# Kernel tuning notes

Hardware: AMD Instinct MI355X
Metric: run time of the kernel (lower is better)

## Reference

```python
import jax, jax.numpy as jnp
import numpy as np

IN_FEATURES = 512
OUT_FEATURES = 512
GRID_MIN = -2.0
GRID_MAX = 2.0
NUM_GRIDS = 8
SPLINE_SCALE = 0.1
BATCH = 16384


def setup_inputs() -> dict:
    key = jax.random.key(0)
    kx, kw = jax.random.split(key)
    x = jax.random.normal(kx, (BATCH, IN_FEATURES), dtype=jnp.float32)
    grid = jnp.linspace(GRID_MIN, GRID_MAX, NUM_GRIDS, dtype=jnp.float32)
    spline_weight = (
        jax.random.normal(kw, (IN_FEATURES * NUM_GRIDS, OUT_FEATURES), dtype=jnp.float32)
        * SPLINE_SCALE
    )
    return {"x": x, "grid": grid, "spline_weight": spline_weight}


def reference(x, grid, spline_weight):
    # denominator h = (grid_max - grid_min) / (num_grids - 1)
    h = (GRID_MAX - GRID_MIN) / (NUM_GRIDS - 1)
    # basis: [B, in_features, num_grids]
    basis = jnp.exp(-jnp.square((x[..., None] - grid) / h))
    # flatten to [B, in_features * num_grids] and GEMM
    return basis.reshape(basis.shape[0], -1) @ spline_weight
```

## Files before the change

### kernel.cpp

```cpp
#include <hip/hip_runtime.h>
#include <hip/hip_bf16.h>

#define BATCH 16384
#define IN_F 512
#define OUT_F 512
#define NG 8
#define KTOT (IN_F * NG)

#define SH    2.1019642153762872f
#define SSTEP 1.2011224087864498f
#define BC0N  4.2039284307525745f
#define RC1   2.4022448175728996f

typedef __attribute__((ext_vector_type(8))) short short8;
typedef __attribute__((ext_vector_type(16))) float f32x16;
typedef __attribute__((ext_vector_type(4))) float f32x4;
typedef __attribute__((ext_vector_type(2))) float f32x2;
typedef __attribute__((ext_vector_type(4))) unsigned int u32x4;
typedef __attribute__((ext_vector_type(2))) unsigned int u32x2;

__device__ __forceinline__ unsigned fbits(float f) {
    union { float f; unsigned u; } v; v.f = f; return v.u;
}
__device__ __forceinline__ unsigned pack2bf(float lo, float hi) {
    return __builtin_amdgcn_perm(fbits(hi) + 0x8000u, fbits(lo) + 0x8000u,
                                 0x07060302u);
}
__device__ __forceinline__ unsigned cvtpk(float lo, float hi) {
    unsigned r;
    asm("v_cvt_pk_bf16_f32 %0, %1, %2" : "=v"(r) : "v"(lo), "v"(hi));
    return r;
}

__device__ __forceinline__ short8 basis_frag(float x) {
    const float t0  = fmaf(x, SH, BC0N);
    const float rho = __builtin_amdgcn_exp2f(t0 * RC1);
    const float v0  = __builtin_amdgcn_exp2f(-t0 * t0);
    const float v1 = v0 * rho;
    const float v2 = v1 * rho;
    const float v3 = v2 * rho;
    const float v4 = v3 * rho;
    const float v5 = v4 * rho;
    const float v6 = v5 * rho;
    const float v7 = v6 * rho;
    u32x4 pk;
    pk[0] = cvtpk(v0, v1);
    pk[1] = cvtpk(v2, v3);
    pk[2] = cvtpk(v4, v5);
    pk[3] = cvtpk(v6, v7);
    union { u32x4 u; short8 s; } cv; cv.u = pk;
    return cv.s;
}

__global__ void prep14(const float* __restrict__ W, const float* __restrict__ X,
                       unsigned short* __restrict__ Wt32, float* __restrict__ XtF32) {
    const int tid = threadIdx.x;
    if (blockIdx.x < 1024) {
        const int gid  = blockIdx.x * 256 + tid;
        const int lane = gid & 63;
        const int t    = (gid >> 6) & 255;
        const int s32  = gid >> 14;
        const int n    = s32 * 32 + (lane & 31);
        const int k0   = t * 16 + (lane >> 5) * 8;
        constexpr float QS[8] = {1.0f,
                                 3.6787944117144233e-1f,
                                 1.8315638888734179e-2f,
                                 1.2340980408667956e-4f,
                                 1.1253517471925912e-7f,
                                 1.3887943864964021e-11f,
                                 2.3195228302435693e-16f,
                                 5.2428856633634640e-22f};
        u32x4 pk;
#pragma unroll
        for (int e = 0; e < 4; ++e)
            pk[e] = pack2bf(W[(size_t)(k0 + 2 * e) * OUT_F + n] * QS[2 * e],
                            W[(size_t)(k0 + 2 * e + 1) * OUT_F + n] * QS[2 * e + 1]);
        *(u32x4*)(Wt32 + (size_t)gid * 8) = pk;
    } else {
        __shared__ float ls[64][36];
        const int bid2 = blockIdx.x - 1024;
        const int rb   = bid2 >> 4;
        const int g    = bid2 & 15;
        const int m0   = rb * 64;
        const int c0   = g * 32;
#pragma unroll
        for (int p = 0; p < 2; ++p) {
            const int idx  = p * 1024 + tid * 4;
            const int row  = idx >> 5;
            const int col4 = idx & 31;
            f32x4 v = *(const f32x4*)(X + (size_t)(m0 + row) * IN_F + c0 + col4);
            *(f32x4*)(&ls[row][col4]) = v;
        }
        __syncthreads();
#pragma unroll
        for (int q = 0; q < 4; ++q) {
            const int p    = q * 256 + tid;
            const int th   = p >> 6;
            const int lane = p & 63;
            const int col  = th * 2 + (lane >> 5);
            f32x2 v;
            v.x = ls[lane & 31][col];
            v.y = ls[(lane & 31) + 32][col];
            *(f32x2*)(XtF32 + ((size_t)(rb * 256 + g * 16 + th) * 64 + lane) * 2) = v;
        }
    }
}

__global__ __launch_bounds__(256, 2) void gauss_gemm14(
        const float* __restrict__ XtF32, const unsigned short* __restrict__ Wt32,
        float* __restrict__ Out) {
    const int tid  = threadIdx.x;
    const int lane = tid & 63;
    const int wave = tid >> 6;
    const int nb = (blockIdx.x & 7) * 64 + (blockIdx.x >> 3);
    const int cb = nb >> 8;
    const int rb = nb & 255;
    const int m0 = rb * 64;
    const int n0 = cb * 256;
    const int s64 = cb * 4 + wave;
    const int s32a = s64 * 2, s32b = s64 * 2 + 1;

    const unsigned short* bp0 = Wt32 + (size_t)s32a * 131072 + lane * 8;
    const unsigned short* bp1 = Wt32 + (size_t)s32b * 131072 + lane * 8;
    const float* ap = XtF32 + (size_t)rb * 32768 + lane * 2;

    f32x16 c00 = {0.f}, c01 = {0.f}, c10 = {0.f}, c11 = {0.f};
#pragma unroll
    for (int e = 0; e < 16; ++e) { c00[e] = 0.f; c01[e] = 0.f; c10[e] = 0.f; c11[e] = 0.f; }

    short8 b0C, b1C, b0N, b1N;
    f32x2 xC, xN;

    xC  = *(const f32x2*)(ap);
    b0C = *(const short8*)(bp0);
    b1C = *(const short8*)(bp1);

#define GG14(XU, B0U, B1U, XF, B0F, B1F, DOFF)                                 \
    {                                                                          \
        XF  = *(const f32x2*)(ap + (DOFF) * 128);                              \
        B0F = *(const short8*)(bp0 + (DOFF) * 512);                            \
        B1F = *(const short8*)(bp1 + (DOFF) * 512);                            \
        const short8 a0 = basis_frag(XU.x);                                    \
        const short8 a1 = basis_frag(XU.y);                                    \
        __builtin_amdgcn_s_setprio(1);                                         \
        c00 = __builtin_amdgcn_mfma_f32_32x32x16_bf16(a0, B0U, c00, 0, 0, 0);  \
        c01 = __builtin_amdgcn_mfma_f32_32x32x16_bf16(a0, B1U, c01, 0, 0, 0);  \
        c10 = __builtin_amdgcn_mfma_f32_32x32x16_bf16(a1, B0U, c10, 0, 0, 0);  \
        c11 = __builtin_amdgcn_mfma_f32_32x32x16_bf16(a1, B1U, c11, 0, 0, 0);  \
        __builtin_amdgcn_s_setprio(0);                                         \
    }

    for (int m = 0; m < 127; ++m) {
        GG14(xC, b0C, b1C, xN, b0N, b1N, 1)
        GG14(xN, b0N, b1N, xC, b0C, b1C, 2)
        ap  += 256;
        bp0 += 1024;
        bp1 += 1024;
    }
    GG14(xC, b0C, b1C, xN, b0N, b1N, 1)
    {
        const short8 a0 = basis_frag(xN.x);
        const short8 a1 = basis_frag(xN.y);
        __builtin_amdgcn_s_setprio(1);
        c00 = __builtin_amdgcn_mfma_f32_32x32x16_bf16(a0, b0N, c00, 0, 0, 0);
        c01 = __builtin_amdgcn_mfma_f32_32x32x16_bf16(a0, b1N, c01, 0, 0, 0);
        c10 = __builtin_amdgcn_mfma_f32_32x32x16_bf16(a1, b0N, c10, 0, 0, 0);
        c11 = __builtin_amdgcn_mfma_f32_32x32x16_bf16(a1, b1N, c11, 0, 0, 0);
        __builtin_amdgcn_s_setprio(0);
    }
#undef GG14

    const int ccol = lane & 31;
    const int rof  = 4 * (lane >> 5);
#pragma unroll
    for (int e = 0; e < 16; ++e) {
        const int row = (e & 3) + 8 * (e >> 2) + rof;
        const int c0c = n0 + wave * 64 + ccol;
        Out[(size_t)(m0 + row) * OUT_F + c0c]            = c00[e];
        Out[(size_t)(m0 + row) * OUT_F + c0c + 32]       = c01[e];
        Out[(size_t)(m0 + 32 + row) * OUT_F + c0c]       = c10[e];
        Out[(size_t)(m0 + 32 + row) * OUT_F + c0c + 32]  = c11[e];
    }
}

#define BM 128
#define BN 128
#define BK 64
#define LDA 72
#define LDB 72

__global__ __launch_bounds__(256, 2) void gauss_gemm_fb(
        const float* __restrict__ X, const float* __restrict__ W,
        float* __restrict__ Out) {
    __shared__ __align__(16) unsigned short sA[BM * LDA];
    __shared__ __align__(16) unsigned short sB2[BN * LDB];

    const int tid  = threadIdx.x;
    const int lane = tid & 63;
    const int wave = tid >> 6;
    const int rb = blockIdx.x >> 2;
    const int cbx = blockIdx.x & 3;
    const int m0 = rb * BM;
    const int n0 = cbx * BN;
    const int wr = (wave >> 1) * 64;
    const int wc = (wave & 1) * 64;
    const int l15 = lane & 15;
    const int lq  = lane >> 4;

    f32x4 acc[4][4];
#pragma unroll
    for (int i = 0; i < 4; ++i)
#pragma unroll
        for (int j = 0; j < 4; ++j)
            acc[i][j] = (f32x4){0.f, 0.f, 0.f, 0.f};

    const int arow = tid & 127;
    const int axq  = tid >> 7;

    for (int kt = 0; kt < KTOT / BK; ++kt) {
        const int k0  = kt * BK;
        const int xc0 = kt * (BK / NG);

        const f32x4 xv = *(const f32x4*)(X + (size_t)(m0 + arow) * IN_F + xc0 + 4 * axq);
        unsigned short* sArow = sA + arow * LDA + axq * 32;
#pragma unroll
        for (int j = 0; j < 4; ++j) {
            const float xs = xv[j] * SH;
            u32x4 pk;
#pragma unroll
            for (int g = 0; g < 8; g += 2) {
                float t0 = xs + (BC0N - g * SSTEP);
                float t1 = xs + (BC0N - (g + 1) * SSTEP);
                pk[g >> 1] = pack2bf(__builtin_amdgcn_exp2f(-t0 * t0),
                                     __builtin_amdgcn_exp2f(-t1 * t1));
            }
            *(u32x4*)(sArow + j * 8) = pk;
        }

#pragma unroll
        for (int p = 0; p < 8; ++p) {
            int id = p * 256 + tid;
            int n  = id & 127;
            int k4 = id >> 7;
            const float* wp = W + (size_t)(k0 + k4 * 4) * OUT_F + n0 + n;
            u32x2 v;
            v[0] = pack2bf(wp[0], wp[OUT_F]);
            v[1] = pack2bf(wp[2 * OUT_F], wp[3 * OUT_F]);
            *(u32x2*)(sB2 + n * LDB + k4 * 4) = v;
        }

        __syncthreads();

#pragma unroll
        for (int kk = 0; kk < BK; kk += 32) {
            short8 af[4], bfv[4];
#pragma unroll
            for (int i = 0; i < 4; ++i)
                af[i] = *(const short8*)(sA + (wr + i * 16 + l15) * LDA + kk + lq * 8);
#pragma unroll
            for (int i = 0; i < 4; ++i)
                bfv[i] = *(const short8*)(sB2 + (wc + i * 16 + l15) * LDB + kk + lq * 8);
#pragma unroll
            for (int i = 0; i < 4; ++i)
#pragma unroll
                for (int j = 0; j < 4; ++j)
                    acc[i][j] = __builtin_amdgcn_mfma_f32_16x16x32_bf16(af[i], bfv[j], acc[i][j], 0, 0, 0);
        }

        __syncthreads();
    }

#pragma unroll
    for (int i = 0; i < 4; ++i) {
        const int r0 = m0 + wr + i * 16 + lq * 4;
#pragma unroll
        for (int j = 0; j < 4; ++j) {
            const int c = n0 + wc + j * 16 + l15;
#pragma unroll
            for (int e = 0; e < 4; ++e)
                Out[(size_t)(r0 + e) * OUT_F + c] = acc[i][j][e];
        }
    }
}

extern "C" void kernel_launch(void* const* d_in, const int* in_sizes, int n_in,
                              void* d_out, int out_size, void* d_ws, size_t ws_size,
                              hipStream_t stream) {
    (void)in_sizes; (void)n_in; (void)out_size;
    const float* X = (const float*)d_in[0];
    const float* W = (const float*)d_in[2];
    float* Out = (float*)d_out;

    const size_t xtf_bytes = (size_t)BATCH * IN_F * sizeof(float);
    const size_t wt_bytes  = (size_t)KTOT * OUT_F * sizeof(unsigned short);
    if (ws_size >= xtf_bytes + wt_bytes) {
        float* XtF32 = (float*)d_ws;
        unsigned short* Wt32 = (unsigned short*)((char*)d_ws + xtf_bytes);
        prep14<<<dim3(1024 + 4096), 256, 0, stream>>>(W, X, Wt32, XtF32);
        gauss_gemm14<<<dim3((BATCH / 64) * (OUT_F / 256)), 256, 0, stream>>>(XtF32, Wt32, Out);
    } else {
        gauss_gemm_fb<<<dim3((BATCH / BM) * (OUT_F / BN)), 256, 0, stream>>>(X, W, Out);
    }
}
```

Baseline: 170.2 us.

## Deepen GEMM register prefetch to four stages and tile weight prep through LDS

The main GEMM loop now keeps four K-steps of X and weight fragments in flight in registers instead of two, so global loads are issued further ahead of the MFMAs that use them. The basis computation multiplies by rho squared to shorten the serial multiply chain, and it uses the HIP bf16x2 conversion intrinsic instead of inline asm. The weight-prep kernel now stages 64x64 tiles through shared memory so its global reads are coalesced, replacing the strided per-element loads. The deeper prefetch raises register pressure under launch_bounds(256,2), which could cause spills or lower occupancy.

```diff
diff --git a/kernel.cpp b/kernel.cpp
--- a/kernel.cpp
+++ b/kernel.cpp
@@ -26,42 +26,39 @@
     return __builtin_amdgcn_perm(fbits(hi) + 0x8000u, fbits(lo) + 0x8000u,
                                  0x07060302u);
 }
-__device__ __forceinline__ unsigned cvtpk(float lo, float hi) {
-    unsigned r;
-    asm("v_cvt_pk_bf16_f32 %0, %1, %2" : "=v"(r) : "v"(lo), "v"(hi));
-    return r;
-}
-
-__device__ __forceinline__ short8 basis_frag(float x) {
+
+__device__ __forceinline__ short8 basis_frag2(float x) {
     const float t0  = fmaf(x, SH, BC0N);
     const float rho = __builtin_amdgcn_exp2f(t0 * RC1);
     const float v0  = __builtin_amdgcn_exp2f(-t0 * t0);
+    const float r2  = rho * rho;
     const float v1 = v0 * rho;
-    const float v2 = v1 * rho;
-    const float v3 = v2 * rho;
-    const float v4 = v3 * rho;
-    const float v5 = v4 * rho;
-    const float v6 = v5 * rho;
-    const float v7 = v6 * rho;
-    u32x4 pk;
-    pk[0] = cvtpk(v0, v1);
-    pk[1] = cvtpk(v2, v3);
-    pk[2] = cvtpk(v4, v5);
-    pk[3] = cvtpk(v6, v7);
-    union { u32x4 u; short8 s; } cv; cv.u = pk;
-    return cv.s;
-}
-
-__global__ void prep14(const float* __restrict__ W, const float* __restrict__ X,
+    const float v2 = v0 * r2, v3 = v1 * r2;
+    const float v4 = v2 * r2, v5 = v3 * r2;
+    const float v6 = v4 * r2, v7 = v5 * r2;
+    union { __hip_bfloat162 h[4]; short8 s; } u;
+    u.h[0] = __float22bfloat162_rn(make_float2(v0, v1));
+    u.h[1] = __float22bfloat162_rn(make_float2(v2, v3));
+    u.h[2] = __float22bfloat162_rn(make_float2(v4, v5));
+    u.h[3] = __float22bfloat162_rn(make_float2(v6, v7));
+    return u.s;
+}
+
+__global__ void prep15(const float* __restrict__ W, const float* __restrict__ X,
                        unsigned short* __restrict__ Wt32, float* __restrict__ XtF32) {
+    __shared__ float lsf[64 * 68];
     const int tid = threadIdx.x;
-    if (blockIdx.x < 1024) {
-        const int gid  = blockIdx.x * 256 + tid;
-        const int lane = gid & 63;
-        const int t    = (gid >> 6) & 255;
-        const int s32  = gid >> 14;
-        const int n    = s32 * 32 + (lane & 31);
-        const int k0   = t * 16 + (lane >> 5) * 8;
+    if (blockIdx.x < 512) {
+        const int kg = blockIdx.x & 63;
+        const int ng = blockIdx.x >> 6;
+#pragma unroll
+        for (int p = 0; p < 4; ++p) {
+            const int row = p * 16 + (tid >> 4);
+            const int c4  = (tid & 15) * 4;
+            f32x4 v = *(const f32x4*)(W + (size_t)(kg * 64 + row) * OUT_F + ng * 64 + c4);
+            *(f32x4*)(&lsf[row * 68 + c4]) = v;
+        }
+        __syncthreads();
         constexpr float QS[8] = {1.0f,
                                  3.6787944117144233e-1f,
                                  1.8315638888734179e-2f,
@@ -70,15 +67,26 @@
                                  1.3887943864964021e-11f,
                                  2.3195228302435693e-16f,
                                  5.2428856633634640e-22f};
-        u32x4 pk;
-#pragma unroll
-        for (int e = 0; e < 4; ++e)
-            pk[e] = pack2bf(W[(size_t)(k0 + 2 * e) * OUT_F + n] * QS[2 * e],
-                            W[(size_t)(k0 + 2 * e + 1) * OUT_F + n] * QS[2 * e + 1]);
-        *(u32x4*)(Wt32 + (size_t)gid * 8) = pk;
+#pragma unroll
+        for (int it = 0; it < 2; ++it) {
+            const int item = it * 256 + tid;
+            const int sl   = item >> 8;
+            const int th   = (item >> 6) & 3;
+            const int lane = item & 63;
+            const int kb   = th * 16 + (lane >> 5) * 8;
+            const int nc   = sl * 32 + (lane & 31);
+            union { __hip_bfloat162 h[4]; u32x4 u; } pk;
+#pragma unroll
+            for (int e = 0; e < 4; ++e)
+                pk.h[e] = __float22bfloat162_rn(make_float2(
+                    lsf[(kb + 2 * e) * 68 + nc] * QS[2 * e],
+                    lsf[(kb + 2 * e + 1) * 68 + nc] * QS[2 * e + 1]));
+            const int s32 = 2 * ng + sl;
+            const int t   = kg * 4 + th;
+            *(u32x4*)(Wt32 + ((size_t)(s32 * 256 + t) * 64 + lane) * 8) = pk.u;
+        }
     } else {
-        __shared__ float ls[64][36];
-        const int bid2 = blockIdx.x - 1024;
+        const int bid2 = blockIdx.x - 512;
         const int rb   = bid2 >> 4;
         const int g    = bid2 & 15;
         const int m0   = rb * 64;
@@ -89,7 +97,7 @@
             const int row  = idx >> 5;
             const int col4 = idx & 31;
             f32x4 v = *(const f32x4*)(X + (size_t)(m0 + row) * IN_F + c0 + col4);
-            *(f32x4*)(&ls[row][col4]) = v;
+            *(f32x4*)(&lsf[row * 36 + col4]) = v;
         }
         __syncthreads();
 #pragma unroll
@@ -99,14 +107,14 @@
             const int lane = p & 63;
             const int col  = th * 2 + (lane >> 5);
             f32x2 v;
-            v.x = ls[lane & 31][col];
-            v.y = ls[(lane & 31) + 32][col];
+            v.x = lsf[(lane & 31) * 36 + col];
+            v.y = lsf[((lane & 31) + 32) * 36 + col];
             *(f32x2*)(XtF32 + ((size_t)(rb * 256 + g * 16 + th) * 64 + lane) * 2) = v;
         }
     }
 }
 
-__global__ __launch_bounds__(256, 2) void gauss_gemm14(
+__global__ __launch_bounds__(256, 2) void gauss_gemm15(
         const float* __restrict__ XtF32, const unsigned short* __restrict__ Wt32,
         float* __restrict__ Out) {
     const int tid  = threadIdx.x;
@@ -124,51 +132,63 @@
     const unsigned short* bp1 = Wt32 + (size_t)s32b * 131072 + lane * 8;
     const float* ap = XtF32 + (size_t)rb * 32768 + lane * 2;
 
-    f32x16 c00 = {0.f}, c01 = {0.f}, c10 = {0.f}, c11 = {0.f};
+    f32x16 c00, c01, c10, c11;
 #pragma unroll
     for (int e = 0; e < 16; ++e) { c00[e] = 0.f; c01[e] = 0.f; c10[e] = 0.f; c11[e] = 0.f; }
 
-    short8 b0C, b1C, b0N, b1N;
-    f32x2 xC, xN;
-
-    xC  = *(const f32x2*)(ap);
-    b0C = *(const short8*)(bp0);
-    b1C = *(const short8*)(bp1);
-
-#define GG14(XU, B0U, B1U, XF, B0F, B1F, DOFF)                                 \
+    f32x2 xa0, xa1, xa2, xa3;
+    short8 b0_0, b0_1, b0_2, b0_3, b1_0, b1_1, b1_2, b1_3;
+
+    xa0 = *(const f32x2*)(ap);        b0_0 = *(const short8*)(bp0);
+    b1_0 = *(const short8*)(bp1);
+    xa1 = *(const f32x2*)(ap + 128);  b0_1 = *(const short8*)(bp0 + 512);
+    b1_1 = *(const short8*)(bp1 + 512);
+    xa2 = *(const f32x2*)(ap + 256);  b0_2 = *(const short8*)(bp0 + 1024);
+    b1_2 = *(const short8*)(bp1 + 1024);
+    xa3 = *(const f32x2*)(ap + 384);  b0_3 = *(const short8*)(bp0 + 1536);
+    b1_3 = *(const short8*)(bp1 + 1536);
+
+#define STEP15(K)                                                              \
     {                                                                          \
-        XF  = *(const f32x2*)(ap + (DOFF) * 128);                              \
-        B0F = *(const short8*)(bp0 + (DOFF) * 512);                            \
-        B1F = *(const short8*)(bp1 + (DOFF) * 512);                            \
-        const short8 a0 = basis_frag(XU.x);                                    \
-        const short8 a1 = basis_frag(XU.y);                                    \
+        const short8 a0 = basis_frag2(xa##K.x);                                \
+        const short8 a1 = basis_frag2(xa##K.y);                                \
+        xa##K = *(const f32x2*)(ap + (K) * 128);                               \
         __builtin_amdgcn_s_setprio(1);                                         \
-        c00 = __builtin_amdgcn_mfma_f32_32x32x16_bf16(a0, B0U, c00, 0, 0, 0);  \
-        c01 = __builtin_amdgcn_mfma_f32_32x32x16_bf16(a0, B1U, c01, 0, 0, 0);  \
-        c10 = __builtin_amdgcn_mfma_f32_32x32x16_bf16(a1, B0U, c10, 0, 0, 0);  \
-        c11 = __builtin_amdgcn_mfma_f32_32x32x16_bf16(a1, B1U, c11, 0, 0, 0);  \
+        c00 = __builtin_amdgcn_mfma_f32_32x32x16_bf16(a0, b0_##K, c00, 0,0,0); \
+        c01 = __builtin_amdgcn_mfma_f32_32x32x16_bf16(a0, b1_##K, c01, 0,0,0); \
+        c10 = __builtin_amdgcn_mfma_f32_32x32x16_bf16(a1, b0_##K, c10, 0,0,0); \
+        c11 = __builtin_amdgcn_mfma_f32_32x32x16_bf16(a1, b1_##K, c11, 0,0,0); \
         __builtin_amdgcn_s_setprio(0);                                         \
-    }
-
-    for (int m = 0; m < 127; ++m) {
-        GG14(xC, b0C, b1C, xN, b0N, b1N, 1)
-        GG14(xN, b0N, b1N, xC, b0C, b1C, 2)
-        ap  += 256;
-        bp0 += 1024;
-        bp1 += 1024;
-    }
-    GG14(xC, b0C, b1C, xN, b0N, b1N, 1)
-    {
-        const short8 a0 = basis_frag(xN.x);
-        const short8 a1 = basis_frag(xN.y);
-        __builtin_amdgcn_s_setprio(1);
-        c00 = __builtin_amdgcn_mfma_f32_32x32x16_bf16(a0, b0N, c00, 0, 0, 0);
-        c01 = __builtin_amdgcn_mfma_f32_32x32x16_bf16(a0, b1N, c01, 0, 0, 0);
-        c10 = __builtin_amdgcn_mfma_f32_32x32x16_bf16(a1, b0N, c10, 0, 0, 0);
-        c11 = __builtin_amdgcn_mfma_f32_32x32x16_bf16(a1, b1N, c11, 0, 0, 0);
-        __builtin_amdgcn_s_setprio(0);
-    }
-#undef GG14
+        b0_##K = *(const short8*)(bp0 + (K) * 512);                            \
+        b1_##K = *(const short8*)(bp1 + (K) * 512);                            \
+    }
+#define TSTEP15(K)                                                             \
+    {                                                                          \
+        const short8 a0 = basis_frag2(xa##K.x);                                \
+        const short8 a1 = basis_frag2(xa##K.y);                                \
+        __builtin_amdgcn_s_setprio(1);                                         \
+        c00 = __builtin_amdgcn_mfma_f32_32x32x16_bf16(a0, b0_##K, c00, 0,0,0); \
+        c01 = __builtin_amdgcn_mfma_f32_32x32x16_bf16(a0, b1_##K, c01, 0,0,0); \
+        c10 = __builtin_amdgcn_mfma_f32_32x32x16_bf16(a1, b0_##K, c10, 0,0,0); \
+        c11 = __builtin_amdgcn_mfma_f32_32x32x16_bf16(a1, b1_##K, c11, 0,0,0); \
+        __builtin_amdgcn_s_setprio(0);                                         \
+    }
+
+    for (int t4 = 1; t4 < 64; ++t4) {
+        ap  += 512;
+        bp0 += 2048;
+        bp1 += 2048;
+        STEP15(0)
+        STEP15(1)
+        STEP15(2)
+        STEP15(3)
+    }
+    TSTEP15(0)
+    TSTEP15(1)
+    TSTEP15(2)
+    TSTEP15(3)
+#undef STEP15
+#undef TSTEP15
 
     const int ccol = lane & 31;
     const int rof  = 4 * (lane >> 5);
@@ -296,8 +316,8 @@
     if (ws_size >= xtf_bytes + wt_bytes) {
         float* XtF32 = (float*)d_ws;
         unsigned short* Wt32 = (unsigned short*)((char*)d_ws + xtf_bytes);
-        prep14<<<dim3(1024 + 4096), 256, 0, stream>>>(W, X, Wt32, XtF32);
-        gauss_gemm14<<<dim3((BATCH / 64) * (OUT_F / 256)), 256, 0, stream>>>(XtF32, Wt32, Out);
+        prep15<<<dim3(512 + 4096), 256, 0, stream>>>(W, X, Wt32, XtF32);
+        gauss_gemm15<<<dim3((BATCH / 64) * (OUT_F / 256)), 256, 0, stream>>>(XtF32, Wt32, Out);
     } else {
         gauss_gemm_fb<<<dim3((BATCH / BM) * (OUT_F / BN)), 256, 0, stream>>>(X, W, Out);
     }
```

Result: slower. 184.5 us (+8.4%).
